# Kernel optimization log

Measured on AMD Instinct MI355X. Metric: run time of the kernel, lower is better.

Reference implementation:

```python
import jax, jax.numpy as jnp
import numpy as np

# SoftNMS hyperparameters (init_kwargs)
IOU_THRESHOLD = 0.5     # only used for method='linear'
SIGMA = 0.5
SCORE_THRESHOLD = 0.001
METHOD = 'gaussian'

N_BOXES = 4096
NUM_CLASSES = 2


def setup_inputs() -> dict:
    key = jax.random.key(0)
    k1, k2, k3, k4 = jax.random.split(key, 4)
    # valid boxes: corner in [0,1000), size in [8,96) -> realistic overlaps
    xy = jax.random.uniform(k1, (N_BOXES, 2), minval=0.0, maxval=1000.0)
    wh = jax.random.uniform(k2, (N_BOXES, 2), minval=8.0, maxval=96.0)
    boxes = jnp.concatenate([xy, xy + wh], axis=1)  # [N,4] x1,y1,x2,y2
    scores = jax.random.uniform(k3, (N_BOXES,), minval=0.05, maxval=1.0)
    labels = jax.random.randint(k4, (N_BOXES,), 0, NUM_CLASSES)
    return {"boxes": boxes, "scores": scores, "labels": labels}


def _iou_one_vs_all(box, boxes):
    # box: [4], boxes: [N,4] -> iou [N]
    lt = jnp.maximum(box[:2], boxes[:, :2])
    rb = jnp.minimum(box[2:], boxes[:, 2:])
    wh = jnp.clip(rb - lt, 0.0)
    inter = wh[:, 0] * wh[:, 1]
    a1 = (box[2] - box[0]) * (box[3] - box[1])
    a2 = (boxes[:, 2] - boxes[:, 0]) * (boxes[:, 3] - boxes[:, 1])
    return inter / (a1 + a2 - inter + 1e-8)


def _soft_nms(boxes, scores, labels):
    # Vectorized soft-NMS. Classes are processed jointly: decay only couples
    # boxes of the SAME class, so interleaving classes by global argmax is
    # mathematically identical to the per-class while-loop of the original.
    N = boxes.shape[0]

    def step(carry, _):
        cur, active = carry  # cur: decayed scores [N], active: bool [N]
        masked = jnp.where(active, cur, -jnp.inf)
        i = jnp.argmax(masked)
        valid = jnp.any(active)
        sel_box = boxes[i]
        ious = _iou_one_vs_all(sel_box, boxes)  # [N]
        same_cls = (labels == labels[i]) & active
        if METHOD == 'linear':
            decay = jnp.where(ious > IOU_THRESHOLD, 1.0 - ious, jnp.ones_like(ious))
        else:
            decay = jnp.exp(-(ious ** 2) / SIGMA)
        new = jnp.where(same_cls, cur * decay, cur)
        new_active = active & (new >= SCORE_THRESHOLD)
        new_active = new_active.at[i].set(False)
        # if nothing is active anymore, keep state frozen
        new_active = jnp.where(valid, new_active, active)
        new = jnp.where(valid, new, cur)
        sel_score = jnp.where(valid, cur[i], 0.0)
        return (new, new_active), (i, sel_score, valid)

    init = (scores, jnp.ones((N,), dtype=bool))
    (_, _), (idx, sel_scores, valid) = jax.lax.scan(step, init, None, length=N)
    v = valid.astype(boxes.dtype)
    sel_boxes = boxes[idx] * v[:, None]          # [N,4], zeroed where invalid
    sel_scores = sel_scores * v                  # [N]
    sel_labels = jnp.where(valid, labels[idx], -1)  # [N], -1 = padding
    return sel_boxes, sel_scores, sel_labels


def reference(boxes, scores, labels):
    return _soft_nms(boxes, scores, labels)
```

## Files before the change

kernel.cpp:

```cpp
#include <hip/hip_runtime.h>
#include <stdint.h>


#define N_BOXES 4096
#define T 512
#define NWAVE (T / 64)
#define CAP 8
#define FOLD (T / 64)
#define BOXCAP 2560
#define SCORE_THR 0.001f
#define BMAX 32

typedef unsigned long long u64;
typedef uint32_t u32;

__device__ __forceinline__ u64 kmax(u64 a, u64 b) { return a > b ? a : b; }
__device__ __forceinline__ u64 kmin(u64 a, u64 b) { return a < b ? a : b; }

__device__ __forceinline__ int wave_max_nonneg(int v) {
    v = max(v, __builtin_amdgcn_update_dpp(0, v, 0x111, 0xf, 0xf, false));
    v = max(v, __builtin_amdgcn_update_dpp(0, v, 0x112, 0xf, 0xf, false));
    v = max(v, __builtin_amdgcn_update_dpp(0, v, 0x114, 0xf, 0xf, false));
    v = max(v, __builtin_amdgcn_update_dpp(0, v, 0x118, 0xf, 0xf, false));
    v = max(v, __builtin_amdgcn_update_dpp(0, v, 0x142, 0xa, 0xf, false));
    v = max(v, __builtin_amdgcn_update_dpp(0, v, 0x143, 0xc, 0xf, false));
    return __builtin_amdgcn_readlane(v, 63);
}

__device__ __forceinline__ u64 wave_max_u64(u64 x) {
    int hi   = (int)(u32)(x >> 32);
    int hmax = wave_max_nonneg(hi);
    int lom  = (hi == hmax) ? (int)(u32)x : 0;
    int lmax = wave_max_nonneg(lom);
    return ((u64)(u32)hmax << 32) | (u64)(u32)lmax;
}

__device__ __forceinline__ float readlane_f(float v, int l) {
    return __uint_as_float((u32)__builtin_amdgcn_readlane((int)__float_as_uint(v), l));
}
__device__ __forceinline__ u64 readlane_u64(u64 v, int l) {
    u32 lo = (u32)__builtin_amdgcn_readlane((int)(u32)(v & 0xFFFFFFFFull), l);
    u32 hi = (u32)__builtin_amdgcn_readlane((int)(u32)(v >> 32), l);
    return ((u64)hi << 32) | (u64)lo;
}
__device__ __forceinline__ u64 shflxor64(u64 v, int m) {
    int lo = __shfl_xor((int)(u32)(v & 0xFFFFFFFFull), m, 64);
    int hi = __shfl_xor((int)(u32)(v >> 32), m, 64);
    return ((u64)(u32)hi << 32) | (u64)(u32)lo;
}

#define WS_KEY(ws, c)  ((u64*)((char*)(ws) + (size_t)(c) * 32768))
#define WS_BOX(ws, c)  ((float4*)((char*)(ws) + 65536 + (size_t)(c) * 65536))
#define WS_CNT(ws)     ((int*)((char*)(ws) + 196608))

__launch_bounds__(T, 1)
__global__ void softnms_fused(const float* __restrict__ boxes,
                              const float* __restrict__ scores,
                              const int* __restrict__ labels,
                              void* __restrict__ ws) {
    const int cls  = blockIdx.x;
    const int tid  = threadIdx.x;
    const int lane = tid & 63;
    const int wid  = tid >> 6;

    __shared__ u64    maskw[64];
    __shared__ u32    wordpref[64];
    __shared__ u64    redG[NWAVE];
    __shared__ u64    cand[T];
    __shared__ float4 batchbox[BMAX];
    __shared__ u32    batchstat[BMAX];
    __shared__ float4 box_lds[BOXCAP];
    __shared__ u64    okey_lds[BOXCAP];

    for (int base = 0; base < N_BOXES; base += T) {
        u64 bal = __ballot(labels[base + tid] == cls);
        if (lane == 0) maskw[(base >> 6) + wid] = bal;
    }
    __syncthreads();
    if (wid == 0) {
        u32 v = (u32)__popcll(maskw[lane]);
        #pragma unroll
        for (int d = 1; d < 64; d <<= 1) {
            u32 o = __shfl_up(v, d, 64);
            if (lane >= d) v += o;
        }
        wordpref[lane] = v;
    }
    __syncthreads();
    const int cnt = __builtin_amdgcn_readfirstlane((int)wordpref[63]);

    float x1r[CAP], y1r[CAP], x2r[CAP], y2r[CAP], ar[CAP];
    u64 key[CAP];
    const float4* boxes4 = reinterpret_cast<const float4*>(boxes);
    #pragma unroll
    for (int j = 0; j < CAP; ++j) {
        key[j] = 0;
        x1r[j] = 0.0f; y1r[j] = 0.0f; x2r[j] = 0.0f; y2r[j] = 0.0f; ar[j] = 0.0f;
        int r = tid + T * j;
        if (r < cnt) {
            int lo = 0, hi = 63;
            while (lo < hi) { int mid = (lo + hi) >> 1; if (wordpref[mid] > (u32)r) hi = mid; else lo = mid + 1; }
            int W = lo;
            u32 rb = (W == 0) ? 0u : wordpref[W - 1];
            u32 t = (u32)r - rb;
            u64 x = maskw[W];
            int pos = 0;
            u32 c;
            c = (u32)__popcll(x & 0xFFFFFFFFull); if (t >= c) { pos += 32; t -= c; x >>= 32; }
            c = (u32)__popcll(x & 0xFFFFull);     if (t >= c) { pos += 16; t -= c; x >>= 16; }
            c = (u32)__popcll(x & 0xFFull);       if (t >= c) { pos += 8;  t -= c; x >>= 8; }
            c = (u32)__popcll(x & 0xFull);        if (t >= c) { pos += 4;  t -= c; x >>= 4; }
            c = (u32)__popcll(x & 0x3ull);        if (t >= c) { pos += 2;  t -= c; x >>= 2; }
            c = (u32)__popcll(x & 0x1ull);        if (t >= c) { pos += 1; }
            int g = W * 64 + pos;
            float4 b = boxes4[g];
            x1r[j] = b.x; y1r[j] = b.y; x2r[j] = b.z; y2r[j] = b.w;
            ar[j]  = __fmul_rn(__fsub_rn(b.z, b.x), __fsub_rn(b.w, b.y));
            float s = scores[g];
            key[j] = ((u64)__float_as_uint(s) << 32)
                   | ((u64)(u32)(4095 - g) << 16) | (u64)(u32)r;
            if (r < BOXCAP) box_lds[r] = b;
        }
    }
    __syncthreads();

    u64*    okey = WS_KEY(ws, cls);
    float4* obox = WS_BOX(ws, cls);
    const bool use_lds = (cnt <= BOXCAP);
    int mcnt = 0;

    for (int outer = 0; outer <= N_BOXES; ++outer) {
        u64 m1 = 0, m2 = 0;
        #pragma unroll
        for (int j = 0; j < CAP; ++j) {
            if (T * j < cnt) {
                u64 kj  = key[j];
                u64 nm1 = kmax(m1, kj);
                m2 = kmax(m2, kmin(m1, kj));
                m1 = nm1;
            }
        }
        u64 wg = wave_max_u64(m2);
        if (lane == 0) redG[wid] = wg;
        cand[tid] = m1;
        __syncthreads();

        u64 c1 = 0, c2 = 0;
        #pragma unroll
        for (int q = 0; q < FOLD; ++q) {
            u64 c  = cand[lane + 64 * q];
            u64 n1 = kmax(c1, c);
            c2 = kmax(c2, kmin(c1, c));
            c1 = n1;
        }
        u64 Gr = redG[0];
        #pragma unroll
        for (int q = 1; q < NWAVE; ++q) Gr = kmax(Gr, redG[q]);
        u64 G = kmax(Gr, wave_max_u64(c2));

        u64 val = c1;
        #pragma unroll
        for (int kk = 2; kk <= 64; kk <<= 1) {
            #pragma unroll
            for (int jj = kk >> 1; jj > 0; jj >>= 1) {
                u64 o = shflxor64(val, jj);
                bool up    = (lane & kk) != 0;
                bool lower = (lane & jj) == 0;
                u64 mn = kmin(val, o), mx = kmax(val, o);
                val = (lower == up) ? mn : mx;
            }
        }
        bool clean = (val != 0);

        float4 cbx;
        if (use_lds) cbx = box_lds[(int)(val & 0xFFFF)];
        else         cbx = boxes4[4095 - (int)((val >> 16) & 0xFFFF)];
        float carX = __fmul_rn(__fsub_rn(cbx.z, cbx.x), __fsub_rn(cbx.w, cbx.y));

        u64 dirtyTop = 0;

        u32 hm[CAP];
        #pragma unroll
        for (int j = 0; j < CAP; ++j) hm[j] = 0;

        int did = 0;
        for (;;) {
            u64 cleanMask = __ballot(clean);
            u64 cleanTop = 0;
            if (cleanMask != 0)
                cleanTop = readlane_u64(val, (int)__builtin_ctzll(cleanMask));
            u64 w = kmax(cleanTop, dirtyTop);
            if (w == 0) break;
            if (w <= G) break;
            if (did == BMAX) break;
            bool fromClean = (w == cleanTop);

            u64 wb = __ballot(val == w);
            int wlane = (int)__builtin_ctzll(wb);
            float wx1 = readlane_f(cbx.x, wlane);
            float wy1 = readlane_f(cbx.y, wlane);
            float wx2 = readlane_f(cbx.z, wlane);
            float wy2 = readlane_f(cbx.w, wlane);
            float warea = readlane_f(carX, wlane);

            if (tid == 0) {
                batchbox[did]  = make_float4(wx1, wy1, wx2, wy2);
                batchstat[did] = (u32)w;
                if (use_lds) { if (mcnt < BOXCAP) okey_lds[mcnt] = w; }
                else if (mcnt < N_BOXES) { okey[mcnt] = w; obox[mcnt] = make_float4(wx1, wy1, wx2, wy2); }
            }

            float ix1 = fmaxf(wx1, cbx.x);
            float iy1 = fmaxf(wy1, cbx.y);
            float ix2 = fminf(wx2, cbx.z);
            float iy2 = fminf(wy2, cbx.w);
            float iw  = fmaxf(__fsub_rn(ix2, ix1), 0.0f);
            float ih  = fmaxf(__fsub_rn(iy2, iy1), 0.0f);
            float inter = __fmul_rn(iw, ih);
            bool ov = (inter > 0.0f) & (val != 0) & (lane != wlane);
            u64 ob = __ballot(ov);

            if (lane == wlane) { val = 0; clean = false; }

            if (ob != 0) {
                float den = __fadd_rn(__fsub_rn(__fadd_rn(warea, carX), inter), 1e-8f);
                float iou = inter / den;
                float d   = expf(__fmul_rn(-2.0f, __fmul_rn(iou, iou)));
                float sc  = __uint_as_float((u32)(val >> 32));
                float ns  = __fmul_rn(sc, d);
                u64   nv  = ((u64)__float_as_uint(ns) << 32) | (val & 0xFFFFFFFFull);
                if (ov) { val = (ns >= SCORE_THR) ? nv : 0; clean = false; }
            }
            if (ob != 0 || !fromClean) {
                u64 dv = (!clean && val != 0) ? val : 0;
                dirtyTop = wave_max_u64(dv);
            }

            u32 bit = 1u << did;
            #pragma unroll
            for (int j = 0; j < CAP; ++j) {
                if (T * j < cnt) {
                    bool hit = (wx2 > x1r[j]) & (x2r[j] > wx1)
                             & (wy2 > y1r[j]) & (y2r[j] > wy1);
                    hm[j] = hit ? (hm[j] | bit) : hm[j];
                }
            }
            mcnt++; did++;
        }
        if (did == 0) break;
        __syncthreads();

        #pragma unroll
        for (int j = 0; j < CAP; ++j) {
            if (T * j < cnt) {
                u32 m = hm[j];
                while (m) {
                    int b = (int)__builtin_ctz(m);
                    m &= (m - 1);
                    float4 wbx = batchbox[b];
                    u32   wst = batchstat[b];
                    float wx1 = wbx.x, wy1 = wbx.y, wx2 = wbx.z, wy2 = wbx.w;
                    float warea = __fmul_rn(__fsub_rn(wx2, wx1), __fsub_rn(wy2, wy1));
                    u64 kj = key[j];
                    float ix1   = fmaxf(wx1, x1r[j]);
                    float iy1   = fmaxf(wy1, y1r[j]);
                    float ix2   = fminf(wx2, x2r[j]);
                    float iy2   = fminf(wy2, y2r[j]);
                    float iw    = fmaxf(__fsub_rn(ix2, ix1), 0.0f);
                    float ih    = fmaxf(__fsub_rn(iy2, iy1), 0.0f);
                    float inter = __fmul_rn(iw, ih);
                    float denom = __fadd_rn(__fsub_rn(__fadd_rn(warea, ar[j]), inter), 1e-8f);
                    float iou   = inter / denom;
                    float t2    = __fmul_rn(iou, iou);
                    float decay = expf(__fmul_rn(-2.0f, t2));
                    float sc    = __uint_as_float((u32)(kj >> 32));
                    float ns    = __fmul_rn(sc, decay);
                    bool  app   = (kj != 0) && (inter > 0.0f);
                    u64   nk    = ((u64)__float_as_uint(ns) << 32) | (kj & 0xFFFFFFFFull);
                    u64   upd   = app ? ((ns >= SCORE_THR) ? nk : 0ull) : kj;
                    key[j] = ((u32)kj == wst) ? 0ull : upd;
                }
            }
        }
    }

    int mfin = (mcnt <= cnt) ? mcnt : cnt;
    if (use_lds) {
        __syncthreads();
        int fl = (mfin <= BOXCAP) ? mfin : BOXCAP;
        for (int m = tid; m < fl; m += T) {
            u64 w = okey_lds[m];
            okey[m] = w;
            obox[m] = box_lds[(int)(w & 0xFFFF)];
        }
    }
    if (tid == 0) WS_CNT(ws)[cls] = mfin;
}

__global__ void softnms_merge(void* __restrict__ ws, float* __restrict__ out) {
    int k = blockIdx.x * blockDim.x + threadIdx.x;
    const u64*    keyA = WS_KEY(ws, 0);
    const u64*    keyB = WS_KEY(ws, 1);
    const float4* boxA = WS_BOX(ws, 0);
    const float4* boxB = WS_BOX(ws, 1);
    const int mA = WS_CNT(ws)[0];
    const int mB = WS_CNT(ws)[1];

    float* ob = out;
    float* os = out + N_BOXES * 4;
    float* ol = out + N_BOXES * 5;

    if (k < mA) {
        u64 x = keyA[k];
        int lo = 0, hi = mB;
        while (lo < hi) { int mid = (lo + hi) >> 1; if (keyB[mid] > x) lo = mid + 1; else hi = mid; }
        int pos = k + lo;
        float4 b = boxA[k];
        ob[pos * 4 + 0] = b.x; ob[pos * 4 + 1] = b.y;
        ob[pos * 4 + 2] = b.z; ob[pos * 4 + 3] = b.w;
        os[pos] = __uint_as_float((u32)(x >> 32));
        ol[pos] = 0.0f;
    } else if (k < mA + mB) {
        int i = k - mA;
        u64 x = keyB[i];
        int lo = 0, hi = mA;
        while (lo < hi) { int mid = (lo + hi) >> 1; if (keyA[mid] > x) lo = mid + 1; else hi = mid; }
        int pos = i + lo;
        float4 b = boxB[i];
        ob[pos * 4 + 0] = b.x; ob[pos * 4 + 1] = b.y;
        ob[pos * 4 + 2] = b.z; ob[pos * 4 + 3] = b.w;
        os[pos] = __uint_as_float((u32)(x >> 32));
        ol[pos] = 1.0f;
    } else {
        ob[k * 4 + 0] = 0.0f; ob[k * 4 + 1] = 0.0f;
        ob[k * 4 + 2] = 0.0f; ob[k * 4 + 3] = 0.0f;
        os[k] = 0.0f;
        ol[k] = -1.0f;
    }
}

extern "C" void kernel_launch(void* const* d_in, const int* in_sizes, int n_in,
                              void* d_out, int out_size, void* d_ws, size_t ws_size,
                              hipStream_t stream) {
    const float* boxes  = (const float*)d_in[0];
    const float* scores = (const float*)d_in[1];
    const int*   labels = (const int*)d_in[2];
    float* out = (float*)d_out;
    (void)in_sizes; (void)n_in; (void)out_size; (void)ws_size;
    softnms_fused<<<2, T, 0, stream>>>(boxes, scores, labels, d_ws);
    softnms_merge<<<N_BOXES / 256, 256, 0, stream>>>(d_ws, out);
}
```

Baseline: 2.323 ms.

## Select up to four non-overlapping winners per round without bitonic sort

The per-round bitonic sort of 64 candidate keys and the clean/dirty tracking are removed. The wave now picks up to KD=4 successive maxima directly with DPP max reductions, and stops at the first pick whose box overlaps an earlier pick. Because the picks are mutually disjoint, their decays on the candidates and the batch hit masks are applied in a single pass. This is meant to cut per-winner cross-lane reduction and shuffle latency in the serial selection loop. In exchange it adds register arrays, a tie-breaking path on the low key word, and a stricter stop on the first overlapping winner.

```diff
diff --git a/kernel.cpp b/kernel.cpp
--- a/kernel.cpp
+++ b/kernel.cpp
@@ -10,6 +10,7 @@
 #define BOXCAP 2560
 #define SCORE_THR 0.001f
 #define BMAX 32
+#define KD 4
 
 typedef unsigned long long u64;
 typedef uint32_t u32;
@@ -37,16 +38,6 @@
 
 __device__ __forceinline__ float readlane_f(float v, int l) {
     return __uint_as_float((u32)__builtin_amdgcn_readlane((int)__float_as_uint(v), l));
-}
-__device__ __forceinline__ u64 readlane_u64(u64 v, int l) {
-    u32 lo = (u32)__builtin_amdgcn_readlane((int)(u32)(v & 0xFFFFFFFFull), l);
-    u32 hi = (u32)__builtin_amdgcn_readlane((int)(u32)(v >> 32), l);
-    return ((u64)hi << 32) | (u64)lo;
-}
-__device__ __forceinline__ u64 shflxor64(u64 v, int m) {
-    int lo = __shfl_xor((int)(u32)(v & 0xFFFFFFFFull), m, 64);
-    int hi = __shfl_xor((int)(u32)(v >> 32), m, 64);
-    return ((u64)(u32)hi << 32) | (u64)(u32)lo;
 }
 
 #define WS_KEY(ws, c)  ((u64*)((char*)(ws) + (size_t)(c) * 32768))
@@ -157,27 +148,14 @@
         #pragma unroll
         for (int q = 1; q < NWAVE; ++q) Gr = kmax(Gr, redG[q]);
         u64 G = kmax(Gr, wave_max_u64(c2));
-
-        u64 val = c1;
-        #pragma unroll
-        for (int kk = 2; kk <= 64; kk <<= 1) {
-            #pragma unroll
-            for (int jj = kk >> 1; jj > 0; jj >>= 1) {
-                u64 o = shflxor64(val, jj);
-                bool up    = (lane & kk) != 0;
-                bool lower = (lane & jj) == 0;
-                u64 mn = kmin(val, o), mx = kmax(val, o);
-                val = (lower == up) ? mn : mx;
-            }
-        }
-        bool clean = (val != 0);
-
-        float4 cbx;
-        if (use_lds) cbx = box_lds[(int)(val & 0xFFFF)];
-        else         cbx = boxes4[4095 - (int)((val >> 16) & 0xFFFF)];
-        float carX = __fmul_rn(__fsub_rn(cbx.z, cbx.x), __fsub_rn(cbx.w, cbx.y));
-
-        u64 dirtyTop = 0;
+        const u32 Ghi = (u32)(G >> 32), Glo = (u32)G;
+
+        u32 cscb = (u32)(c1 >> 32);
+        u32 cst  = (u32)c1;
+        float4 cb;
+        if (use_lds) cb = box_lds[(int)(c1 & 0xFFFF)];
+        else         cb = boxes4[4095 - (int)((c1 >> 16) & 0xFFFF)];
+        float car = __fmul_rn(__fsub_rn(cb.z, cb.x), __fsub_rn(cb.w, cb.y));
 
         u32 hm[CAP];
         #pragma unroll
@@ -185,67 +163,118 @@
 
         int did = 0;
         for (;;) {
-            u64 cleanMask = __ballot(clean);
-            u64 cleanTop = 0;
-            if (cleanMask != 0)
-                cleanTop = readlane_u64(val, (int)__builtin_ctzll(cleanMask));
-            u64 w = kmax(cleanTop, dirtyTop);
-            if (w == 0) break;
-            if (w <= G) break;
-            if (did == BMAX) break;
-            bool fromClean = (w == cleanTop);
-
-            u64 wb = __ballot(val == w);
-            int wlane = (int)__builtin_ctzll(wb);
-            float wx1 = readlane_f(cbx.x, wlane);
-            float wy1 = readlane_f(cbx.y, wlane);
-            float wx2 = readlane_f(cbx.z, wlane);
-            float wy2 = readlane_f(cbx.w, wlane);
-            float warea = readlane_f(carX, wlane);
+            u32 wuh[KD], wul[KD]; int wsrc[KD];
+            float wx1[KD], wy1[KD], wx2[KD], wy2[KD], war[KD];
+            int nw = 0;
+            u32 mcs = cscb;
+            bool cont = true;
+            #pragma unroll
+            for (int t = 0; t < KD; ++t) {
+                if (cont && (did + t) < BMAX) {
+                    int h = wave_max_nonneg((int)mcs);
+                    u32 uh = (u32)h;
+                    bool found = (uh != 0u) && (uh >= Ghi);
+                    u32 ul = 0; int src = 0;
+                    if (found) {
+                        u64 bm = __ballot(mcs == uh);
+                        if (__popcll(bm) == 1) {
+                            src = (int)__builtin_ctzll(bm);
+                            ul  = (u32)__builtin_amdgcn_readlane((int)cst, src);
+                        } else {
+                            int lom = (mcs == uh) ? (int)cst : 0;
+                            ul = (u32)wave_max_nonneg(lom);
+                            src = (int)__builtin_ctzll(__ballot((mcs == uh) & (cst == ul)));
+                        }
+                        if (uh == Ghi && ul <= Glo) found = false;
+                    }
+                    if (found) {
+                        float bx1 = readlane_f(cb.x, src);
+                        float by1 = readlane_f(cb.y, src);
+                        float bx2 = readlane_f(cb.z, src);
+                        float by2 = readlane_f(cb.w, src);
+                        float ba  = readlane_f(car,  src);
+                        bool ok = true;
+                        #pragma unroll
+                        for (int p = 0; p < KD; ++p) {
+                            if (p < t) {
+                                bool ovl = (wx2[p] > bx1) & (bx2 > wx1[p])
+                                         & (wy2[p] > by1) & (by2 > wy1[p]);
+                                ok &= !ovl;
+                            }
+                        }
+                        if (ok) {
+                            wuh[t] = uh; wul[t] = ul; wsrc[t] = src;
+                            wx1[t] = bx1; wy1[t] = by1;
+                            wx2[t] = bx2; wy2[t] = by2; war[t] = ba;
+                            mcs = (lane == src) ? 0u : mcs;
+                            nw = t + 1;
+                        } else {
+                            cont = false;
+                        }
+                    } else {
+                        cont = false;
+                    }
+                } else {
+                    cont = false;
+                }
+            }
+            if (nw == 0) break;
 
             if (tid == 0) {
-                batchbox[did]  = make_float4(wx1, wy1, wx2, wy2);
-                batchstat[did] = (u32)w;
-                if (use_lds) { if (mcnt < BOXCAP) okey_lds[mcnt] = w; }
-                else if (mcnt < N_BOXES) { okey[mcnt] = w; obox[mcnt] = make_float4(wx1, wy1, wx2, wy2); }
-            }
-
-            float ix1 = fmaxf(wx1, cbx.x);
-            float iy1 = fmaxf(wy1, cbx.y);
-            float ix2 = fminf(wx2, cbx.z);
-            float iy2 = fminf(wy2, cbx.w);
-            float iw  = fmaxf(__fsub_rn(ix2, ix1), 0.0f);
-            float ih  = fmaxf(__fsub_rn(iy2, iy1), 0.0f);
-            float inter = __fmul_rn(iw, ih);
-            bool ov = (inter > 0.0f) & (val != 0) & (lane != wlane);
-            u64 ob = __ballot(ov);
-
-            if (lane == wlane) { val = 0; clean = false; }
-
-            if (ob != 0) {
-                float den = __fadd_rn(__fsub_rn(__fadd_rn(warea, carX), inter), 1e-8f);
-                float iou = inter / den;
-                float d   = expf(__fmul_rn(-2.0f, __fmul_rn(iou, iou)));
-                float sc  = __uint_as_float((u32)(val >> 32));
-                float ns  = __fmul_rn(sc, d);
-                u64   nv  = ((u64)__float_as_uint(ns) << 32) | (val & 0xFFFFFFFFull);
-                if (ov) { val = (ns >= SCORE_THR) ? nv : 0; clean = false; }
-            }
-            if (ob != 0 || !fromClean) {
-                u64 dv = (!clean && val != 0) ? val : 0;
-                dirtyTop = wave_max_u64(dv);
-            }
-
-            u32 bit = 1u << did;
+                #pragma unroll
+                for (int t = 0; t < KD; ++t) {
+                    if (t < nw) {
+                        u64 wk = ((u64)wuh[t] << 32) | (u64)wul[t];
+                        float4 wb4 = make_float4(wx1[t], wy1[t], wx2[t], wy2[t]);
+                        batchbox[did + t]  = wb4;
+                        batchstat[did + t] = wul[t];
+                        if (use_lds) { if (mcnt + t < BOXCAP) okey_lds[mcnt + t] = wk; }
+                        else if (mcnt + t < N_BOXES) { okey[mcnt + t] = wk; obox[mcnt + t] = wb4; }
+                    }
+                }
+            }
+
+            float s = __uint_as_float(cscb);
+            #pragma unroll
+            for (int t = 0; t < KD; ++t) {
+                if (t < nw) {
+                    float ix1 = fmaxf(wx1[t], cb.x);
+                    float iy1 = fmaxf(wy1[t], cb.y);
+                    float ix2 = fminf(wx2[t], cb.z);
+                    float iy2 = fminf(wy2[t], cb.w);
+                    float iw  = fmaxf(__fsub_rn(ix2, ix1), 0.0f);
+                    float ih  = fmaxf(__fsub_rn(iy2, iy1), 0.0f);
+                    float itr = __fmul_rn(iw, ih);
+                    u64 obt = __ballot((itr > 0.0f) & (lane != wsrc[t]));
+                    if (obt != 0) {
+                        float den = __fadd_rn(__fsub_rn(__fadd_rn(war[t], car), itr), 1e-8f);
+                        float iou = itr / den;
+                        float d   = expf(__fmul_rn(-2.0f, __fmul_rn(iou, iou)));
+                        float n   = __fmul_rn(s, d);
+                        float k   = (n >= SCORE_THR) ? n : 0.0f;
+                        s = (itr > 0.0f) ? k : s;
+                    }
+                    s = (lane == wsrc[t]) ? 0.0f : s;
+                }
+            }
+            cscb = __float_as_uint(s);
+
             #pragma unroll
             for (int j = 0; j < CAP; ++j) {
                 if (T * j < cnt) {
-                    bool hit = (wx2 > x1r[j]) & (x2r[j] > wx1)
-                             & (wy2 > y1r[j]) & (y2r[j] > wy1);
-                    hm[j] = hit ? (hm[j] | bit) : hm[j];
-                }
-            }
-            mcnt++; did++;
+                    u32 hb = 0;
+                    #pragma unroll
+                    for (int t = 0; t < KD; ++t) {
+                        if (t < nw) {
+                            bool hit = (wx2[t] > x1r[j]) & (x2r[j] > wx1[t])
+                                     & (wy2[t] > y1r[j]) & (y2r[j] > wy1[t]);
+                            hb |= hit ? (1u << (did + t)) : 0u;
+                        }
+                    }
+                    hm[j] |= hb;
+                }
+            }
+            mcnt += nw; did += nw;
         }
         if (did == 0) break;
         __syncthreads();
@@ -257,15 +286,15 @@
                 while (m) {
                     int b = (int)__builtin_ctz(m);
                     m &= (m - 1);
-                    float4 wbx = batchbox[b];
+                    float4 wb = batchbox[b];
                     u32   wst = batchstat[b];
-                    float wx1 = wbx.x, wy1 = wbx.y, wx2 = wbx.z, wy2 = wbx.w;
-                    float warea = __fmul_rn(__fsub_rn(wx2, wx1), __fsub_rn(wy2, wy1));
+                    float wx1b = wb.x, wy1b = wb.y, wx2b = wb.z, wy2b = wb.w;
+                    float warea = __fmul_rn(__fsub_rn(wx2b, wx1b), __fsub_rn(wy2b, wy1b));
                     u64 kj = key[j];
-                    float ix1   = fmaxf(wx1, x1r[j]);
-                    float iy1   = fmaxf(wy1, y1r[j]);
-                    float ix2   = fminf(wx2, x2r[j]);
-                    float iy2   = fminf(wy2, y2r[j]);
+                    float ix1   = fmaxf(wx1b, x1r[j]);
+                    float iy1   = fmaxf(wy1b, y1r[j]);
+                    float ix2   = fminf(wx2b, x2r[j]);
+                    float iy2   = fminf(wy2b, y2r[j]);
                     float iw    = fmaxf(__fsub_rn(ix2, ix1), 0.0f);
                     float ih    = fmaxf(__fsub_rn(iy2, iy1), 0.0f);
                     float inter = __fmul_rn(iw, ih);
```

After: 2.259 ms. 1.03x faster.
